# Kernel optimization log

Hardware: AMD Instinct MI355X
Metric: run time of the kernel (lower is better)

Reference implementation:

```python
import jax, jax.numpy as jnp
import numpy as np
import math

EMBED_DIM = 256
KV_IN_DIM = 64
NUM_HEADS = 1
HEAD_DIM = EMBED_DIM // NUM_HEADS
ROPE_THETA = 10000.0


def rope_angles(end_x, end_y, dim, theta):
    # matches compute_axial_cis: axial (x,y) rotary angles, [end_x*end_y, dim//2]
    n = dim // 4
    f = 1.0 / (theta ** (np.arange(0, dim, 4)[:n].astype(np.float64) / dim))
    t = np.arange(end_x * end_y)
    tx = (t % end_x).astype(np.float64)
    ty = (t // end_x).astype(np.float64)
    ang = np.concatenate([np.outer(tx, f), np.outer(ty, f)], axis=-1)
    return (jnp.asarray(np.cos(ang), dtype=jnp.float32),
            jnp.asarray(np.sin(ang), dtype=jnp.float32))


def apply_rope(x, cos, sin):
    # x: [B,H,S,D]; cos/sin: [S,D//2]; complex rotation in real arithmetic
    xs = x.reshape(*x.shape[:-1], -1, 2)
    x0, x1 = xs[..., 0], xs[..., 1]
    o0 = x0 * cos - x1 * sin
    o1 = x0 * sin + x1 * cos
    return jnp.stack([o0, o1], axis=-1).reshape(x.shape)


def setup_inputs() -> dict:
    key = jax.random.key(0)
    ks = jax.random.split(key, 12)
    B, SQ, SK = 2, 4096, 16448
    q = jax.random.normal(ks[0], (B, SQ, EMBED_DIM), dtype=jnp.float32)
    k = jax.random.normal(ks[1], (B, SK, KV_IN_DIM), dtype=jnp.float32)
    v = jax.random.normal(ks[2], (B, SK, KV_IN_DIM), dtype=jnp.float32)
    attn_mask = jax.random.randint(ks[3], (B, SK, 1), 0, 2) > 0
    s_q = 1.0 / math.sqrt(EMBED_DIM)
    s_kv = 1.0 / math.sqrt(KV_IN_DIM)
    wq = jax.random.uniform(ks[4], (EMBED_DIM, EMBED_DIM), jnp.float32, -s_q, s_q)
    bq = jax.random.uniform(ks[5], (EMBED_DIM,), jnp.float32, -s_q, s_q)
    wk = jax.random.uniform(ks[6], (KV_IN_DIM, EMBED_DIM), jnp.float32, -s_kv, s_kv)
    bk = jax.random.uniform(ks[7], (EMBED_DIM,), jnp.float32, -s_kv, s_kv)
    wv = jax.random.uniform(ks[8], (KV_IN_DIM, EMBED_DIM), jnp.float32, -s_kv, s_kv)
    bv = jax.random.uniform(ks[9], (EMBED_DIM,), jnp.float32, -s_kv, s_kv)
    wo = jax.random.uniform(ks[10], (EMBED_DIM, EMBED_DIM), jnp.float32, -s_q, s_q)
    bo = jax.random.uniform(ks[11], (EMBED_DIM,), jnp.float32, -s_q, s_q)
    return {"q": q, "k": k, "v": v, "attn_mask": attn_mask,
            "wq": wq, "bq": bq, "wk": wk, "bk": bk, "wv": wv, "bv": bv,
            "wo": wo, "bo": bo, "num_k_exclude_rope": 64}


def reference(q, k, v, attn_mask, wq, bq, wk, bk, wv, bv, wo, bo, num_k_exclude_rope):
    B, SQ, _ = q.shape
    SK = k.shape[1]
    H, D = NUM_HEADS, HEAD_DIM
    # projections
    qh = (q @ wq + bq).reshape(B, SQ, H, D).transpose(0, 2, 1, 3)  # [B,H,SQ,D]
    kh = (k @ wk + bk).reshape(B, SK, H, D).transpose(0, 2, 1, 3)
    vh = (v @ wv + bv).reshape(B, SK, H, D).transpose(0, 2, 1, 3)
    # rotary encoding
    w = int(math.sqrt(SQ))
    cos, sin = rope_angles(w, w, D, ROPE_THETA)  # [SQ, D//2]
    qh = apply_rope(qh, cos, sin)
    num_k_rope = SK - num_k_exclude_rope
    r = num_k_rope // SQ  # rope_k_repeat: tile freqs over memory frames
    cos_k = jnp.tile(cos, (r, 1))
    sin_k = jnp.tile(sin, (r, 1))
    k_rot = apply_rope(kh[:, :, :num_k_rope], cos_k, sin_k)
    kh = jnp.concatenate([k_rot, kh[:, :, num_k_rope:]], axis=2)
    # masked SDPA; mask True = attend
    m = attn_mask[..., 0][:, None, None, :]  # [B,1,1,SK]
    scale = 1.0 / math.sqrt(D)
    scores = jnp.einsum("bhqd,bhkd->bhqk", qh, kh) * scale
    scores = jnp.where(m, scores, -jnp.inf)
    attn = jax.nn.softmax(scores, axis=-1)
    out = jnp.einsum("bhqk,bhkd->bhqd", attn, vh)
    out = out.transpose(0, 2, 1, 3).reshape(B, SQ, H * D)
    return out @ wo + bo
```

## Files before the change

kernel.cpp:

```cpp
#include <hip/hip_runtime.h>
#include <hip/hip_bf16.h>
#include <stdint.h>


typedef __attribute__((ext_vector_type(8))) short short8;
typedef __attribute__((ext_vector_type(4))) float f4;

__device__ __forceinline__ unsigned short f2bf(float x) {
  union { float f; uint32_t u; } v; v.f = x;
  return (unsigned short)((v.u + 0x7FFFu + ((v.u >> 16) & 1u)) >> 16);
}

__device__ __forceinline__ uint32_t cvtpk(float a, float b) {
  uint32_t r;
  asm("v_cvt_pk_bf16_f32 %0, %1, %2" : "=v"(r) : "v"(a), "v"(b));
  return r;
}

__device__ __forceinline__ void gl_lds16(const void* g, void* l) {
  __builtin_amdgcn_global_load_lds(
      (const __attribute__((address_space(1))) void*)g,
      (__attribute__((address_space(3))) void*)l, 16, 0, 0);
}

__global__ void rope_tab_k(float2* __restrict__ tab) {
  int idx = blockIdx.x * 256 + threadIdx.x;
  int t = idx >> 6, f = idx & 63;
  float freq = __expf(-(float)f * (9.210340371976184f / 64.0f));
  float ang = (float)t * freq;
  tab[idx] = make_float2(cosf(ang), sinf(ang));
}

__global__ void mask_detect_k(const unsigned int* __restrict__ m, int* __restrict__ flag) {
  __shared__ int sI, sF;
  int t = threadIdx.x;
  if (t == 0) { sI = 1; sF = 1; }
  __syncthreads();
  int okI = 1, okF = 1;
  for (int i = t; i < 2048; i += 256) {
    unsigned int w = m[i];
    if (w > 1u) okI = 0;
    if (w != 0u && w != 0x3F800000u) okF = 0;
  }
  if (!okI) atomicAnd(&sI, 0);
  if (!okF) atomicAnd(&sF, 0);
  __syncthreads();
  if (t == 0) flag[0] = sI ? 0 : (sF ? 1 : 2);
}

__device__ __forceinline__ int mask_at(const void* mk, int f, int i) {
  if (f == 0) return ((const int*)mk)[i] != 0;
  if (f == 1) return ((const float*)mk)[i] != 0.0f;
  return ((const unsigned char*)mk)[i] != 0;
}

__global__ void scan_k(const void* __restrict__ mk, const int* __restrict__ flag,
                       int* __restrict__ comp, int* __restrict__ ncomp) {
  __shared__ int sc[256];
  const int b = blockIdx.x, t = threadIdx.x, f = flag[0];
  const int base = b * 16448;
  const int c0 = t * 65, c1 = min(c0 + 65, 16448);
  int c = 0;
  for (int i = c0; i < c1; ++i) c += mask_at(mk, f, base + i);
  sc[t] = c;
  __syncthreads();
  for (int off = 1; off < 256; off <<= 1) {
    int v = (t >= off) ? sc[t - off] : 0;
    __syncthreads();
    sc[t] += v;
    __syncthreads();
  }
  int w = sc[t] - c;
  int* cb = comp + base;
  for (int i = c0; i < c1; ++i)
    if (mask_at(mk, f, base + i)) cb[w++] = i;
  if (t == 255) ncomp[b] = sc[255];
}

__global__ __launch_bounds__(256) void qproj_k(
    const float* __restrict__ q, const float* __restrict__ wq,
    const float* __restrict__ bq, const float2* __restrict__ tab,
    unsigned short* __restrict__ qh) {
  const int c = threadIdx.x;
  const int rb = blockIdx.x * 8;
  float acc[8];
  const float bias = bq[c];
#pragma unroll
  for (int r = 0; r < 8; ++r) acc[r] = bias;
  for (int ch = 0; ch < 4; ++ch) {
    float wreg[64];
#pragma unroll
    for (int j = 0; j < 64; ++j) wreg[j] = wq[(ch * 64 + j) * 256 + c];
#pragma unroll
    for (int r = 0; r < 8; ++r) {
      const float* qr = q + (size_t)(rb + r) * 256 + ch * 64;
      float a = acc[r];
#pragma unroll
      for (int j = 0; j < 64; ++j) a += qr[j] * wreg[j];
      acc[r] = a;
    }
  }
  const int p = c >> 1;
#pragma unroll
  for (int r = 0; r < 8; ++r) {
    int pos = (rb + r) & 4095;
    float2 cs = (p < 64) ? tab[(pos & 63) * 64 + p] : tab[(pos >> 6) * 64 + (p - 64)];
    float v = acc[r];
    float o = __shfl_xor(v, 1);
    float res = v * cs.x + ((c & 1) ? o * cs.y : -o * cs.y);
    qh[(size_t)(rb + r) * 256 + c] = f2bf(res * 0.0625f);
  }
}

__global__ __launch_bounds__(256) void kvproj_k(
    const float* __restrict__ kin, const float* __restrict__ vin,
    const float* __restrict__ wk, const float* __restrict__ bk,
    const float* __restrict__ wv, const float* __restrict__ bv,
    const float2* __restrict__ tab, const int* __restrict__ nker,
    const int* __restrict__ comp, const int* __restrict__ ncomp,
    unsigned short* __restrict__ kh, unsigned short* __restrict__ vt) {
  __shared__ unsigned short vlds[64 * 258];
  const int c = threadIdx.x;
  const int kb = blockIdx.x, b = blockIdx.y, kind = blockIdx.z;
  const int nc = ncomp[b];
  const int pad = (nc + 31) & ~31;
  if (kb * 64 >= pad) return;
  const float* wm = kind ? wv : wk;
  const float bias = (kind ? bv : bk)[c];
  float wreg[64];
#pragma unroll
  for (int j = 0; j < 64; ++j) wreg[j] = wm[j * 256 + c];
  const int nrope = 16448 - nker[0];
  const int* cmp = comp + b * 16448;
  const float* inb = (kind ? vin : kin) + (size_t)b * 16448 * 64;
  const int rmax = min(64, pad - kb * 64);
  for (int r = 0; r < rmax; ++r) {
    const int ci = kb * 64 + r;
    float a = 0.f;
    int oldrow = 0;
    if (ci < nc) {
      oldrow = cmp[ci];
      const float* row = inb + (size_t)oldrow * 64;
      a = bias;
#pragma unroll
      for (int j = 0; j < 64; ++j) a += row[j] * wreg[j];
    }
    if (kind == 0) {
      if (ci < nc && oldrow < nrope) {
        const int pos = oldrow & 4095, p = c >> 1;
        const float2 cs = (p < 64) ? tab[(pos & 63) * 64 + p]
                                   : tab[(pos >> 6) * 64 + (p - 64)];
        const float o = __shfl_xor(a, 1);
        a = a * cs.x + ((c & 1) ? o * cs.y : -o * cs.y);
      }
      const int kk = ci & 31;
      const int rr = ((kk >> 2) & 1) * 16 + (kk >> 3) * 4 + (kk & 3);
      const size_t rowg = (size_t)(ci & ~31) + rr;
      *(unsigned short*)((char*)kh + ((size_t)b * 16448 + rowg) * 512 +
                         ((2 * c) ^ ((rr & 7) << 4))) = f2bf(a);
    } else {
      vlds[r * 258 + c] = f2bf(a);
    }
  }
  if (kind == 1) {
    __syncthreads();
    char* tb = (char*)vt + ((size_t)b * 514 + (size_t)kb * 2) * 16384;
#pragma unroll
    for (int ti = 0; ti < 2; ++ti) {
      union { uint32_t w[16]; uint4 v4[4]; } u;
#pragma unroll
      for (int kk = 0; kk < 32; kk += 2) {
        uint32_t lo = vlds[(ti * 32 + kk) * 258 + c];
        uint32_t hi = vlds[(ti * 32 + kk + 1) * 258 + c];
        u.w[kk >> 1] = lo | (hi << 16);
      }
#pragma unroll
      for (int qd = 0; qd < 4; ++qd)
        *(uint4*)(tb + (size_t)ti * 16384 + c * 64 + qd * 16) = u.v4[qd];
    }
  }
}

__global__ __launch_bounds__(256, 2) void attn_k(
    const unsigned short* __restrict__ qh, const unsigned short* __restrict__ kh,
    const unsigned short* __restrict__ vt, const int* __restrict__ ncomp,
    float* __restrict__ part, int nseg) {
  __shared__ __align__(16) char lds[16384];
  const int tid = threadIdx.x;
  const int w = tid >> 6, ln = tid & 63;
  const int lr = ln & 15, lg = ln >> 4;
  const int segb = blockIdx.x;
  const int qb = blockIdx.y;
  const int seg = segb >> 1, b = segb & 1;
  const int nc = ncomp[b];
  const int ntiles = (nc + 31) >> 5;
  const int t0 = seg * ntiles / nseg;
  const int t1 = (seg + 1) * ntiles / nseg;

  short8 qf[2][8];
  {
    const unsigned short* qr = qh + (size_t)(b * 4096 + qb * 128 + w * 32 + lr) * 256;
#pragma unroll
    for (int g = 0; g < 2; ++g)
#pragma unroll
      for (int kc = 0; kc < 8; ++kc)
        qf[g][kc] = *(const short8*)(qr + g * 16 * 256 + kc * 32 + lg * 8);
  }
  const f4 fz = {0.f, 0.f, 0.f, 0.f};
  f4 acc[2][16];
#pragma unroll
  for (int g = 0; g < 2; ++g)
#pragma unroll
    for (int i = 0; i < 16; ++i) acc[g][i] = fz;
  float m_[2] = {-1e30f, -1e30f}, l_[2] = {0.f, 0.f};

  const int S = (lr & 7) << 4;
  const int s6 = S & 64, Lo = (lg * 16) ^ (S & 48);
  const int baseE = lr * 512 + Lo + s6;
  const int baseO = lr * 512 + Lo + (64 - s6);

  const char* srcK = (const char*)kh + (size_t)b * 16448 * 512 + (size_t)t0 * 16384;
  const char* gV = (const char*)vt + (size_t)b * 514 * 16384 + (size_t)t0 * 16384
                   + lr * 64 + lg * 16;
  const int stoff = tid * 16;

  for (int it = t0; it < t1; ++it) {
    __syncthreads();
#pragma unroll
    for (int r = 0; r < 4; ++r)
      gl_lds16(srcK + r * 4096 + stoff, lds + r * 4096 + stoff);
    srcK += 16384;
    __syncthreads();
    f4 s[2][2] = {{fz, fz}, {fz, fz}};
#pragma unroll
    for (int kc = 0; kc < 8; ++kc) {
      const int off = ((kc & 1) ? baseO : baseE) + (kc >> 1) * 128;
      short8 k0 = *(const short8*)(lds + off);
      short8 k1 = *(const short8*)(lds + off + 8192);
      s[0][0] = __builtin_amdgcn_mfma_f32_16x16x32_bf16(k0, qf[0][kc], s[0][0], 0, 0, 0);
      s[1][0] = __builtin_amdgcn_mfma_f32_16x16x32_bf16(k0, qf[1][kc], s[1][0], 0, 0, 0);
      s[0][1] = __builtin_amdgcn_mfma_f32_16x16x32_bf16(k1, qf[0][kc], s[0][1], 0, 0, 0);
      s[1][1] = __builtin_amdgcn_mfma_f32_16x16x32_bf16(k1, qf[1][kc], s[1][1], 0, 0, 0);
    }
    if (it * 32 + 32 > nc) {
#pragma unroll
      for (int nt = 0; nt < 2; ++nt)
#pragma unroll
        for (int j = 0; j < 4; ++j)
          if (it * 32 + lg * 8 + nt * 4 + j >= nc) {
            s[0][nt][j] = -30000.f; s[1][nt][j] = -30000.f;
          }
    }
    float tm[2];
#pragma unroll
    for (int g = 0; g < 2; ++g) {
      float t = fmaxf(fmaxf(fmaxf(s[g][0][0], s[g][0][1]), fmaxf(s[g][0][2], s[g][0][3])),
                      fmaxf(fmaxf(s[g][1][0], s[g][1][1]), fmaxf(s[g][1][2], s[g][1][3])));
      t = fmaxf(t, __shfl_xor(t, 16));
      t = fmaxf(t, __shfl_xor(t, 32));
      tm[g] = t;
    }
    if (!__all(tm[0] <= m_[0] + 8.f && tm[1] <= m_[1] + 8.f)) {
#pragma unroll
      for (int g = 0; g < 2; ++g) {
        const float mn = fmaxf(m_[g], tm[g]);
        const float sc = __expf(m_[g] - mn);
        m_[g] = mn; l_[g] *= sc;
#pragma unroll
        for (int dt = 0; dt < 16; ++dt)
#pragma unroll
          for (int j = 0; j < 4; ++j) acc[g][dt][j] *= sc;
      }
    }
    short8 pf[2];
#pragma unroll
    for (int g = 0; g < 2; ++g) {
      union { uint32_t u[4]; short8 v; } pk;
      float ts = 0.f;
#pragma unroll
      for (int nt = 0; nt < 2; ++nt)
#pragma unroll
        for (int jj = 0; jj < 4; jj += 2) {
          float e0 = __expf(s[g][nt][jj] - m_[g]);
          float e1 = __expf(s[g][nt][jj + 1] - m_[g]);
          ts += e0 + e1;
          pk.u[nt * 2 + (jj >> 1)] = cvtpk(e0, e1);
        }
      ts += __shfl_xor(ts, 16);
      ts += __shfl_xor(ts, 32);
      l_[g] += ts;
      pf[g] = pk.v;
    }
#pragma unroll
    for (int bt = 0; bt < 4; ++bt) {
      short8 vf[4];
#pragma unroll
      for (int i = 0; i < 4; ++i) vf[i] = *(const short8*)(gV + (bt * 4 + i) * 1024);
#pragma unroll
      for (int dt = 0; dt < 4; ++dt) {
        acc[0][bt * 4 + dt] = __builtin_amdgcn_mfma_f32_16x16x32_bf16(vf[dt], pf[0], acc[0][bt * 4 + dt], 0, 0, 0);
        acc[1][bt * 4 + dt] = __builtin_amdgcn_mfma_f32_16x16x32_bf16(vf[dt], pf[1], acc[1][bt * 4 + dt], 0, 0, 0);
      }
    }
    gV += 16384;
  }
  const int qrow = qb * 128 + w * 32 + lr;
#pragma unroll
  for (int g = 0; g < 2; ++g) {
    float* pp = part + ((size_t)segb * 4096 + qrow + g * 16) * 260;
#pragma unroll
    for (int dt = 0; dt < 16; ++dt) *(f4*)(pp + dt * 16 + lg * 4) = acc[g][dt];
    if (lg == 0) { pp[256] = m_[g]; pp[257] = l_[g]; }
  }
}

__global__ __launch_bounds__(256) void cogemm_k(
    const float* __restrict__ part, int nseg, const float* __restrict__ wo,
    const float* __restrict__ bo, float* __restrict__ out) {
  __shared__ float rows[8][256];
  const int c = threadIdx.x;
  const int rb = blockIdx.x * 8;
  for (int r = 0; r < 8; ++r) {
    const int row = rb + r, b = row >> 12, rl = row & 4095;
    float M = -1e30f;
    for (int s = 0; s < nseg; ++s)
      M = fmaxf(M, part[(size_t)((s * 2 + b) * 4096 + rl) * 260 + 256]);
    float L = 0.f, val = 0.f;
    for (int s = 0; s < nseg; ++s) {
      size_t ix = (size_t)((s * 2 + b) * 4096 + rl) * 260;
      float wf = __expf(part[ix + 256] - M);
      L += part[ix + 257] * wf;
      val += part[ix + c] * wf;
    }
    rows[r][c] = val / L;
  }
  __syncthreads();
  float acc[8];
  const float bias = bo[c];
#pragma unroll
  for (int r = 0; r < 8; ++r) acc[r] = bias;
  for (int ch = 0; ch < 4; ++ch) {
    float wreg[64];
#pragma unroll
    for (int j = 0; j < 64; ++j) wreg[j] = wo[(ch * 64 + j) * 256 + c];
#pragma unroll
    for (int r = 0; r < 8; ++r) {
      const float* ir = &rows[r][ch * 64];
      float a = acc[r];
#pragma unroll
      for (int j = 0; j < 64; ++j) a += ir[j] * wreg[j];
      acc[r] = a;
    }
  }
#pragma unroll
  for (int r = 0; r < 8; ++r) out[(size_t)(rb + r) * 256 + c] = acc[r];
}

extern "C" void kernel_launch(void* const* d_in, const int* in_sizes, int n_in,
                              void* d_out, int out_size, void* d_ws, size_t ws_size,
                              hipStream_t stream) {
  const float* q  = (const float*)d_in[0];
  const float* k  = (const float*)d_in[1];
  const float* v  = (const float*)d_in[2];
  const void*  mk = d_in[3];
  const float* wq = (const float*)d_in[4];
  const float* bq = (const float*)d_in[5];
  const float* wk = (const float*)d_in[6];
  const float* bk = (const float*)d_in[7];
  const float* wv = (const float*)d_in[8];
  const float* bv = (const float*)d_in[9];
  const float* wo = (const float*)d_in[10];
  const float* bo = (const float*)d_in[11];
  const int* nker = (const int*)d_in[12];
  (void)in_sizes; (void)n_in; (void)out_size;

  char* ws = (char*)d_ws;
  size_t off = 0;
  auto alloc = [&](size_t sz) { size_t o = off; off = (off + sz + 255) & ~(size_t)255; return o; };
  const size_t o_tab  = alloc((size_t)64 * 64 * 8);
  const size_t o_qh   = alloc((size_t)8192 * 256 * 2);
  const size_t o_kh   = alloc((size_t)2 * 16448 * 512);
  const size_t o_vt   = alloc((size_t)2 * 514 * 16384);
  const size_t o_cmp  = alloc((size_t)2 * 16448 * 4);
  const size_t o_ncmp = alloc(256);
  const size_t o_flag = alloc(256);
  const size_t o_part = off;
  auto partsz = [](int s) { return (size_t)s * 2 * 4096 * 260 * 4; };
  int nseg = 8;
  while (nseg > 1 && o_part + partsz(nseg) > ws_size) nseg >>= 1;

  float2* tab        = (float2*)(ws + o_tab);
  unsigned short* qh = (unsigned short*)(ws + o_qh);
  unsigned short* kh = (unsigned short*)(ws + o_kh);
  unsigned short* vt = (unsigned short*)(ws + o_vt);
  int* comp          = (int*)(ws + o_cmp);
  int* ncomp         = (int*)(ws + o_ncmp);
  int* flag          = (int*)(ws + o_flag);
  float* part        = (float*)(ws + o_part);

  rope_tab_k<<<dim3(16), dim3(256), 0, stream>>>(tab);
  mask_detect_k<<<dim3(1), dim3(256), 0, stream>>>((const unsigned int*)mk, flag);
  scan_k<<<dim3(2), dim3(256), 0, stream>>>(mk, flag, comp, ncomp);
  qproj_k<<<dim3(1024), dim3(256), 0, stream>>>(q, wq, bq, tab, qh);
  kvproj_k<<<dim3(257, 2, 2), dim3(256), 0, stream>>>(k, v, wk, bk, wv, bv, tab, nker,
                                                      comp, ncomp, kh, vt);
  attn_k<<<dim3(nseg * 2, 32), dim3(256), 0, stream>>>(qh, kh, vt, ncomp, part, nseg);
  cogemm_k<<<dim3(1024), dim3(256), 0, stream>>>(part, nseg, wo, bo, (float*)d_out);
}
```

Before: 391.1 us.

## Stage projection inputs in LDS, split K/V projections, ballot-based mask compaction

```diff
diff --git a/kernel.cpp b/kernel.cpp
--- a/kernel.cpp
+++ b/kernel.cpp
@@ -31,153 +31,235 @@
   tab[idx] = make_float2(cosf(ang), sinf(ang));
 }
 
-__global__ void mask_detect_k(const unsigned int* __restrict__ m, int* __restrict__ flag) {
-  __shared__ int sI, sF;
-  int t = threadIdx.x;
-  if (t == 0) { sI = 1; sF = 1; }
-  __syncthreads();
-  int okI = 1, okF = 1;
-  for (int i = t; i < 2048; i += 256) {
-    unsigned int w = m[i];
-    if (w > 1u) okI = 0;
-    if (w != 0u && w != 0x3F800000u) okF = 0;
-  }
-  if (!okI) atomicAnd(&sI, 0);
-  if (!okF) atomicAnd(&sF, 0);
-  __syncthreads();
-  if (t == 0) flag[0] = sI ? 0 : (sF ? 1 : 2);
-}
-
 __device__ __forceinline__ int mask_at(const void* mk, int f, int i) {
   if (f == 0) return ((const int*)mk)[i] != 0;
   if (f == 1) return ((const float*)mk)[i] != 0.0f;
   return ((const unsigned char*)mk)[i] != 0;
 }
 
-__global__ void scan_k(const void* __restrict__ mk, const int* __restrict__ flag,
-                       int* __restrict__ comp, int* __restrict__ ncomp) {
-  __shared__ int sc[256];
-  const int b = blockIdx.x, t = threadIdx.x, f = flag[0];
+__global__ __launch_bounds__(256) void scan2_k(const void* __restrict__ mk,
+                                               int* __restrict__ comp,
+                                               int* __restrict__ ncomp) {
+  __shared__ int swc[4];
+  __shared__ int sflag;
+  const int b = blockIdx.x, t = threadIdx.x;
+  const int w4 = t >> 6, lane = t & 63;
+  int okI = 1, okF = 1;
+  const unsigned int* mw = (const unsigned int*)mk;
+  for (int i = t; i < 2048; i += 256) {
+    unsigned int x = mw[i];
+    okI &= (x <= 1u);
+    okF &= (x == 0u || x == 0x3F800000u);
+  }
+  okI = __all(okI); okF = __all(okF);
+  if (t == 0) sflag = 3;
+  __syncthreads();
+  if (lane == 0) atomicAnd(&sflag, (okI ? 1 : 0) | (okF ? 2 : 0));
+  __syncthreads();
+  const int f = (sflag & 1) ? 0 : ((sflag & 2) ? 1 : 2);
   const int base = b * 16448;
-  const int c0 = t * 65, c1 = min(c0 + 65, 16448);
-  int c = 0;
-  for (int i = c0; i < c1; ++i) c += mask_at(mk, f, base + i);
-  sc[t] = c;
-  __syncthreads();
-  for (int off = 1; off < 256; off <<= 1) {
-    int v = (t >= off) ? sc[t - off] : 0;
+  int* cb = comp + base;
+  int running = 0;
+  for (int it = 0; it < 65; ++it) {
+    const int i = it * 256 + t;
+    const int pred = (i < 16448) ? mask_at(mk, f, base + i) : 0;
+    const unsigned long long bal = __ballot(pred);
+    if (lane == 0) swc[w4] = __popcll(bal);
     __syncthreads();
-    sc[t] += v;
+    int wpre = 0, tot = 0;
+#pragma unroll
+    for (int ww = 0; ww < 4; ++ww) {
+      int v = swc[ww];
+      tot += v;
+      if (ww < w4) wpre += v;
+    }
+    if (pred)
+      cb[running + wpre + __popcll(bal & ((1ull << lane) - 1ull))] = i;
+    running += tot;
     __syncthreads();
   }
-  int w = sc[t] - c;
-  int* cb = comp + base;
-  for (int i = c0; i < c1; ++i)
-    if (mask_at(mk, f, base + i)) cb[w++] = i;
-  if (t == 255) ncomp[b] = sc[255];
+  if (t == 0) ncomp[b] = running;
 }
 
 __global__ __launch_bounds__(256) void qproj_k(
     const float* __restrict__ q, const float* __restrict__ wq,
     const float* __restrict__ bq, const float2* __restrict__ tab,
     unsigned short* __restrict__ qh) {
+  __shared__ float qs[16][256];
   const int c = threadIdx.x;
-  const int rb = blockIdx.x * 8;
-  float acc[8];
+  const int rb = blockIdx.x * 16;
+#pragma unroll
+  for (int i = 0; i < 4; ++i) {
+    const int idx = i * 256 + c;
+    const int row = idx >> 6, f4i = idx & 63;
+    *(float4*)&qs[row][f4i * 4] =
+        *(const float4*)(q + (size_t)(rb + row) * 256 + f4i * 4);
+  }
+  __syncthreads();
+  float acc[16];
   const float bias = bq[c];
 #pragma unroll
-  for (int r = 0; r < 8; ++r) acc[r] = bias;
+  for (int r = 0; r < 16; ++r) acc[r] = bias;
   for (int ch = 0; ch < 4; ++ch) {
     float wreg[64];
 #pragma unroll
     for (int j = 0; j < 64; ++j) wreg[j] = wq[(ch * 64 + j) * 256 + c];
 #pragma unroll
-    for (int r = 0; r < 8; ++r) {
-      const float* qr = q + (size_t)(rb + r) * 256 + ch * 64;
+    for (int r = 0; r < 16; ++r) {
       float a = acc[r];
 #pragma unroll
-      for (int j = 0; j < 64; ++j) a += qr[j] * wreg[j];
+      for (int j = 0; j < 64; j += 4) {
+        const float4 x = *(const float4*)&qs[r][ch * 64 + j];
+        a += x.x * wreg[j] + x.y * wreg[j + 1] + x.z * wreg[j + 2] + x.w * wreg[j + 3];
+      }
       acc[r] = a;
     }
   }
   const int p = c >> 1;
 #pragma unroll
-  for (int r = 0; r < 8; ++r) {
-    int pos = (rb + r) & 4095;
-    float2 cs = (p < 64) ? tab[(pos & 63) * 64 + p] : tab[(pos >> 6) * 64 + (p - 64)];
-    float v = acc[r];
-    float o = __shfl_xor(v, 1);
-    float res = v * cs.x + ((c & 1) ? o * cs.y : -o * cs.y);
+  for (int r = 0; r < 16; ++r) {
+    const int pos = (rb + r) & 4095;
+    const float2 cs = (p < 64) ? tab[(pos & 63) * 64 + p]
+                               : tab[(pos >> 6) * 64 + (p - 64)];
+    const float v = acc[r];
+    const float o = __shfl_xor(v, 1);
+    const float res = v * cs.x + ((c & 1) ? o * cs.y : -o * cs.y);
     qh[(size_t)(rb + r) * 256 + c] = f2bf(res * 0.0625f);
   }
 }
 
-__global__ __launch_bounds__(256) void kvproj_k(
-    const float* __restrict__ kin, const float* __restrict__ vin,
-    const float* __restrict__ wk, const float* __restrict__ bk,
-    const float* __restrict__ wv, const float* __restrict__ bv,
-    const float2* __restrict__ tab, const int* __restrict__ nker,
-    const int* __restrict__ comp, const int* __restrict__ ncomp,
-    unsigned short* __restrict__ kh, unsigned short* __restrict__ vt) {
-  __shared__ unsigned short vlds[64 * 258];
+__global__ __launch_bounds__(256) void kproj_k(
+    const float* __restrict__ kin, const float* __restrict__ wk,
+    const float* __restrict__ bk, const float2* __restrict__ tab,
+    const int* __restrict__ nker, const int* __restrict__ comp,
+    const int* __restrict__ ncomp, unsigned short* __restrict__ kh) {
+  __shared__ float xs[64][64];
+  __shared__ int rowidx[64];
   const int c = threadIdx.x;
-  const int kb = blockIdx.x, b = blockIdx.y, kind = blockIdx.z;
+  const int kb = blockIdx.x, b = blockIdx.y;
   const int nc = ncomp[b];
   const int pad = (nc + 31) & ~31;
   if (kb * 64 >= pad) return;
-  const float* wm = kind ? wv : wk;
-  const float bias = (kind ? bv : bk)[c];
+  const int* cmp = comp + b * 16448;
+  if (c < 64) rowidx[c] = (kb * 64 + c < nc) ? cmp[kb * 64 + c] : -1;
+  __syncthreads();
+  const float* inb = kin + (size_t)b * 16448 * 64;
+#pragma unroll
+  for (int i = 0; i < 4; ++i) {
+    const int idx = i * 256 + c;
+    const int row = idx >> 4, f4i = idx & 15;
+    const int ri = rowidx[row];
+    float4 v = make_float4(0.f, 0.f, 0.f, 0.f);
+    if (ri >= 0) v = *(const float4*)(inb + (size_t)ri * 64 + f4i * 4);
+    *(float4*)&xs[row][f4i * 4] = v;
+  }
+  __syncthreads();
   float wreg[64];
 #pragma unroll
-  for (int j = 0; j < 64; ++j) wreg[j] = wm[j * 256 + c];
+  for (int j = 0; j < 64; ++j) wreg[j] = wk[j * 256 + c];
+  const float bias = bk[c];
   const int nrope = 16448 - nker[0];
-  const int* cmp = comp + b * 16448;
-  const float* inb = (kind ? vin : kin) + (size_t)b * 16448 * 64;
-  const int rmax = min(64, pad - kb * 64);
-  for (int r = 0; r < rmax; ++r) {
-    const int ci = kb * 64 + r;
-    float a = 0.f;
-    int oldrow = 0;
-    if (ci < nc) {
-      oldrow = cmp[ci];
-      const float* row = inb + (size_t)oldrow * 64;
-      a = bias;
-#pragma unroll
-      for (int j = 0; j < 64; ++j) a += row[j] * wreg[j];
-    }
-    if (kind == 0) {
-      if (ci < nc && oldrow < nrope) {
-        const int pos = oldrow & 4095, p = c >> 1;
+  const int p = c >> 1;
+  for (int r0 = 0; r0 < 64; r0 += 4) {
+    float a0 = bias, a1 = bias, a2 = bias, a3 = bias;
+#pragma unroll
+    for (int j = 0; j < 64; j += 4) {
+      const float4 x0 = *(const float4*)&xs[r0 + 0][j];
+      const float4 x1 = *(const float4*)&xs[r0 + 1][j];
+      const float4 x2 = *(const float4*)&xs[r0 + 2][j];
+      const float4 x3 = *(const float4*)&xs[r0 + 3][j];
+      a0 += x0.x * wreg[j] + x0.y * wreg[j + 1] + x0.z * wreg[j + 2] + x0.w * wreg[j + 3];
+      a1 += x1.x * wreg[j] + x1.y * wreg[j + 1] + x1.z * wreg[j + 2] + x1.w * wreg[j + 3];
+      a2 += x2.x * wreg[j] + x2.y * wreg[j + 1] + x2.z * wreg[j + 2] + x2.w * wreg[j + 3];
+      a3 += x3.x * wreg[j] + x3.y * wreg[j + 1] + x3.z * wreg[j + 2] + x3.w * wreg[j + 3];
+    }
+    float av[4] = {a0, a1, a2, a3};
+#pragma unroll
+    for (int rr = 0; rr < 4; ++rr) {
+      const int row = r0 + rr;
+      const int ci = kb * 64 + row;
+      const int oldrow = rowidx[row];
+      float a = (oldrow >= 0) ? av[rr] : 0.f;
+      if (oldrow >= 0 && oldrow < nrope) {
+        const int pos = oldrow & 4095;
         const float2 cs = (p < 64) ? tab[(pos & 63) * 64 + p]
                                    : tab[(pos >> 6) * 64 + (p - 64)];
         const float o = __shfl_xor(a, 1);
         a = a * cs.x + ((c & 1) ? o * cs.y : -o * cs.y);
       }
       const int kk = ci & 31;
-      const int rr = ((kk >> 2) & 1) * 16 + (kk >> 3) * 4 + (kk & 3);
-      const size_t rowg = (size_t)(ci & ~31) + rr;
+      const int rr2 = ((kk >> 2) & 1) * 16 + (kk >> 3) * 4 + (kk & 3);
+      const size_t rowg = (size_t)(ci & ~31) + rr2;
       *(unsigned short*)((char*)kh + ((size_t)b * 16448 + rowg) * 512 +
-                         ((2 * c) ^ ((rr & 7) << 4))) = f2bf(a);
-    } else {
-      vlds[r * 258 + c] = f2bf(a);
-    }
-  }
-  if (kind == 1) {
-    __syncthreads();
-    char* tb = (char*)vt + ((size_t)b * 514 + (size_t)kb * 2) * 16384;
-#pragma unroll
-    for (int ti = 0; ti < 2; ++ti) {
-      union { uint32_t w[16]; uint4 v4[4]; } u;
-#pragma unroll
-      for (int kk = 0; kk < 32; kk += 2) {
-        uint32_t lo = vlds[(ti * 32 + kk) * 258 + c];
-        uint32_t hi = vlds[(ti * 32 + kk + 1) * 258 + c];
-        u.w[kk >> 1] = lo | (hi << 16);
-      }
-#pragma unroll
-      for (int qd = 0; qd < 4; ++qd)
-        *(uint4*)(tb + (size_t)ti * 16384 + c * 64 + qd * 16) = u.v4[qd];
-    }
+                         ((2 * c) ^ ((rr2 & 7) << 4))) = f2bf(a);
+    }
+  }
+}
+
+__global__ __launch_bounds__(256) void vproj_k(
+    const float* __restrict__ vin, const float* __restrict__ wv,
+    const float* __restrict__ bv, const int* __restrict__ comp,
+    const int* __restrict__ ncomp, unsigned short* __restrict__ vt) {
+  __shared__ float xs[64][64];
+  __shared__ int rowidx[64];
+  __shared__ unsigned short vlds[64 * 258];
+  const int c = threadIdx.x;
+  const int kb = blockIdx.x, b = blockIdx.y;
+  const int nc = ncomp[b];
+  const int pad = (nc + 31) & ~31;
+  if (kb * 64 >= pad) return;
+  const int* cmp = comp + b * 16448;
+  if (c < 64) rowidx[c] = (kb * 64 + c < nc) ? cmp[kb * 64 + c] : -1;
+  __syncthreads();
+  const float* inb = vin + (size_t)b * 16448 * 64;
+#pragma unroll
+  for (int i = 0; i < 4; ++i) {
+    const int idx = i * 256 + c;
+    const int row = idx >> 4, f4i = idx & 15;
+    const int ri = rowidx[row];
+    float4 v = make_float4(0.f, 0.f, 0.f, 0.f);
+    if (ri >= 0) v = *(const float4*)(inb + (size_t)ri * 64 + f4i * 4);
+    *(float4*)&xs[row][f4i * 4] = v;
+  }
+  __syncthreads();
+  float wreg[64];
+#pragma unroll
+  for (int j = 0; j < 64; ++j) wreg[j] = wv[j * 256 + c];
+  const float bias = bv[c];
+  for (int r0 = 0; r0 < 64; r0 += 4) {
+    float a0 = bias, a1 = bias, a2 = bias, a3 = bias;
+#pragma unroll
+    for (int j = 0; j < 64; j += 4) {
+      const float4 x0 = *(const float4*)&xs[r0 + 0][j];
+      const float4 x1 = *(const float4*)&xs[r0 + 1][j];
+      const float4 x2 = *(const float4*)&xs[r0 + 2][j];
+      const float4 x3 = *(const float4*)&xs[r0 + 3][j];
+      a0 += x0.x * wreg[j] + x0.y * wreg[j + 1] + x0.z * wreg[j + 2] + x0.w * wreg[j + 3];
+      a1 += x1.x * wreg[j] + x1.y * wreg[j + 1] + x1.z * wreg[j + 2] + x1.w * wreg[j + 3];
+      a2 += x2.x * wreg[j] + x2.y * wreg[j + 1] + x2.z * wreg[j + 2] + x2.w * wreg[j + 3];
+      a3 += x3.x * wreg[j] + x3.y * wreg[j + 1] + x3.z * wreg[j + 2] + x3.w * wreg[j + 3];
+    }
+    float av[4] = {a0, a1, a2, a3};
+#pragma unroll
+    for (int rr = 0; rr < 4; ++rr) {
+      const int row = r0 + rr;
+      vlds[row * 258 + c] = f2bf((rowidx[row] >= 0) ? av[rr] : 0.f);
+    }
+  }
+  __syncthreads();
+  char* tb = (char*)vt + ((size_t)b * 514 + (size_t)kb * 2) * 16384;
+#pragma unroll
+  for (int ti = 0; ti < 2; ++ti) {
+    union { uint32_t w[16]; uint4 v4[4]; } u;
+#pragma unroll
+    for (int kk = 0; kk < 32; kk += 2) {
+      uint32_t lo = vlds[(ti * 32 + kk) * 258 + c];
+      uint32_t hi = vlds[(ti * 32 + kk + 1) * 258 + c];
+      u.w[kk >> 1] = lo | (hi << 16);
+    }
+#pragma unroll
+    for (int qd = 0; qd < 4; ++qd)
+      *(uint4*)(tb + (size_t)ti * 16384 + c * 64 + qd * 16) = u.v4[qd];
   }
 }
 
@@ -383,7 +465,6 @@
   const size_t o_vt   = alloc((size_t)2 * 514 * 16384);
   const size_t o_cmp  = alloc((size_t)2 * 16448 * 4);
   const size_t o_ncmp = alloc(256);
-  const size_t o_flag = alloc(256);
   const size_t o_part = off;
   auto partsz = [](int s) { return (size_t)s * 2 * 4096 * 260 * 4; };
   int nseg = 8;
@@ -395,15 +476,13 @@
   unsigned short* vt = (unsigned short*)(ws + o_vt);
   int* comp          = (int*)(ws + o_cmp);
   int* ncomp         = (int*)(ws + o_ncmp);
-  int* flag          = (int*)(ws + o_flag);
   float* part        = (float*)(ws + o_part);
 
   rope_tab_k<<<dim3(16), dim3(256), 0, stream>>>(tab);
-  mask_detect_k<<<dim3(1), dim3(256), 0, stream>>>((const unsigned int*)mk, flag);
-  scan_k<<<dim3(2), dim3(256), 0, stream>>>(mk, flag, comp, ncomp);
-  qproj_k<<<dim3(1024), dim3(256), 0, stream>>>(q, wq, bq, tab, qh);
-  kvproj_k<<<dim3(257, 2, 2), dim3(256), 0, stream>>>(k, v, wk, bk, wv, bv, tab, nker,
-                                                      comp, ncomp, kh, vt);
+  scan2_k<<<dim3(2), dim3(256), 0, stream>>>(mk, comp, ncomp);
+  qproj_k<<<dim3(512), dim3(256), 0, stream>>>(q, wq, bq, tab, qh);
+  kproj_k<<<dim3(257, 2), dim3(256), 0, stream>>>(k, wk, bk, tab, nker, comp, ncomp, kh);
+  vproj_k<<<dim3(257, 2), dim3(256), 0, stream>>>(v, wv, bv, comp, ncomp, vt);
   attn_k<<<dim3(nseg * 2, 32), dim3(256), 0, stream>>>(qh, kh, vt, ncomp, part, nseg);
   cogemm_k<<<dim3(1024), dim3(256), 0, stream>>>(part, nseg, wo, bo, (float*)d_out);
 }
```

Result: slower. 441.5 us (+12.9%).
